# Kernel tuning notes

Hardware: AMD Instinct MI355X
Metric: run time of the kernel (lower is better)

Reference implementation:

```python
import jax, jax.numpy as jnp
import numpy as np


def _sum_matrix():
    # [69, 42] mask matrix reproducing compute_sums exactly (incl. bugs):
    # feature k = sum over cells where M[k] == 1, board flattened row-major (6x7).
    M = np.zeros((69, 42), dtype=np.float32)
    m = M.reshape(69, 6, 7)
    # 24 row window sums
    for row in range(6):
        for i in range(4):
            m[row * 4 + i, row, i:i + 4] = 1.0
    # 21 column window sums
    for col in range(7):
        for i in range(3):
            m[24 + col * 3 + i, i:i + 4, col] = 1.0
    # 12 'upward diag' sums: source sums the FULL 4x4 block of the row-flipped
    # board, i.e. original rows (2-off)..(5-off), cols col..col+3.
    for off in range(3):
        for col in range(4):
            m[45 + off * 4 + col, 2 - off:6 - off, col:col + 4] = 1.0
    # 12 'downward diag' sums: allocated but never written in source -> zeros.
    return jnp.asarray(M)


_M = _sum_matrix()  # [69, 42]


def setup_inputs() -> dict:
    key = jax.random.key(0)
    k1, k2, k3 = jax.random.split(key, 3)
    B = 524288
    game_state = jax.random.normal(k1, (B, 42), dtype=jnp.float32)
    W = jax.random.normal(k2, (7, 111), dtype=jnp.float32) * (1.0 / np.sqrt(111.0))
    b = jax.random.normal(k3, (7,), dtype=jnp.float32) * 0.01
    return {"game_state": game_state, "W": W, "b": b}


def reference(game_state, W, b):
    # sums: [B, 69] = all windowed sums as one GEMM against the mask matrix
    sums = game_state @ _M.T
    feats = jnp.concatenate([game_state, sums], axis=1)  # [B, 111]
    return feats @ W.T + b  # [B, 7]
```

## Files before the change

kernel.cpp:

```cpp
#include <hip/hip_runtime.h>


#define NFP 44

__global__ __launch_bounds__(320)
void ddqn_weff(const float* __restrict__ W, float* __restrict__ weff) {
    int tid = threadIdx.x;
    if (tid >= 7 * NFP) return;
    int j  = tid / NFP;
    int dp = tid % NFP;
    float acc = 0.0f;
    if (dp < 42) {
        acc = W[j * 111 + dp];
        int r = dp / 7, c = dp % 7;
        const float* ws = W + j * 111 + 42;
        for (int i = 0; i < 4; ++i)
            if (c >= i && c <= i + 3) acc += ws[r * 4 + i];
        for (int i = 0; i < 3; ++i)
            if (r >= i && r <= i + 3) acc += ws[24 + c * 3 + i];
        for (int off = 0; off < 3; ++off)
            for (int col = 0; col < 4; ++col)
                if (r >= 2 - off && r <= 5 - off && c >= col && c <= col + 3)
                    acc += ws[45 + off * 4 + col];
    }
    weff[tid] = acc;
}

__global__ __launch_bounds__(256)
void ddqn_main(const float* __restrict__ gs,
               const float* __restrict__ weff,
               const float* __restrict__ b,
               float* __restrict__ out) {
    __shared__ float wl[7 * NFP];
    __shared__ float bl[7];
    int t = threadIdx.x;
    for (int i = t; i < 7 * NFP; i += 256) wl[i] = weff[i];
    if (t < 7) bl[t] = b[t];
    __syncthreads();

    size_t gid = (size_t)blockIdx.x * 256 + (size_t)t;

    const float4* src = (const float4*)(gs + gid * 84);
    float xa[NFP], xb[NFP];
    #pragma unroll
    for (int i = 0; i < 21; ++i) {
        float4 v = src[i];
        float vv[4] = {v.x, v.y, v.z, v.w};
        #pragma unroll
        for (int q = 0; q < 4; ++q) {
            int f = i * 4 + q;
            if (f < 42) xa[f] = vv[q];
            else        xb[f - 42] = vv[q];
        }
    }
    xa[42] = xa[43] = 0.0f;
    xb[42] = xb[43] = 0.0f;

    float acc0[7], acc1[7];
    #pragma unroll
    for (int j = 0; j < 7; ++j) { acc0[j] = bl[j]; acc1[j] = bl[j]; }

    #pragma unroll
    for (int d = 0; d < NFP; d += 4) {
        #pragma unroll
        for (int j = 0; j < 7; ++j) {
            const float4 w = *(const float4*)&wl[j * NFP + d];
            acc0[j] += xa[d] * w.x + xa[d + 1] * w.y + xa[d + 2] * w.z + xa[d + 3] * w.w;
            acc1[j] += xb[d] * w.x + xb[d + 1] * w.y + xb[d + 2] * w.z + xb[d + 3] * w.w;
        }
    }

    float2* o = (float2*)(out + gid * 14);
    o[0] = make_float2(acc0[0], acc0[1]);
    o[1] = make_float2(acc0[2], acc0[3]);
    o[2] = make_float2(acc0[4], acc0[5]);
    o[3] = make_float2(acc0[6], acc1[0]);
    o[4] = make_float2(acc1[1], acc1[2]);
    o[5] = make_float2(acc1[3], acc1[4]);
    o[6] = make_float2(acc1[5], acc1[6]);
}

extern "C" void kernel_launch(void* const* d_in, const int* in_sizes, int n_in,
                              void* d_out, int out_size, void* d_ws, size_t ws_size,
                              hipStream_t stream) {
    const float* gs = (const float*)d_in[0];
    const float* W  = (const float*)d_in[1];
    const float* b  = (const float*)d_in[2];
    float* out  = (float*)d_out;
    float* weff = (float*)d_ws;

    ddqn_weff<<<dim3(1), dim3(320), 0, stream>>>(W, weff);

    int B = in_sizes[0] / 42;
    int nthreads = B / 2;
    ddqn_main<<<dim3(nthreads / 256), dim3(256), 0, stream>>>(gs, weff, b, out);
}
```

Measured before the change: 160.4 us.

## Stage input rows through padded LDS tile for coalesced loads, one row per thread

The main kernel now loads a 128-row tile of the input with fully coalesced scalar loads into padded shared memory, then each thread reads its own row from LDS. Previously each thread handled two rows through strided float4 global loads. Weights are read straight from global memory (uniform, likely scalar loads) instead of being staged in shared memory. The aim is better global-load coalescing, at the cost of an extra LDS round trip, scalar 7-float output stores, and small 128-thread blocks.

```diff
diff --git a/kernel.cpp b/kernel.cpp
--- a/kernel.cpp
+++ b/kernel.cpp
@@ -1,83 +1,67 @@
 #include <hip/hip_runtime.h>
 
 
-#define NFP 44
+#define TILE_ROWS 128
+#define ROW_PAD   43
 
 __global__ __launch_bounds__(320)
 void ddqn_weff(const float* __restrict__ W, float* __restrict__ weff) {
     int tid = threadIdx.x;
-    if (tid >= 7 * NFP) return;
-    int j  = tid / NFP;
-    int dp = tid % NFP;
-    float acc = 0.0f;
-    if (dp < 42) {
-        acc = W[j * 111 + dp];
-        int r = dp / 7, c = dp % 7;
-        const float* ws = W + j * 111 + 42;
-        for (int i = 0; i < 4; ++i)
-            if (c >= i && c <= i + 3) acc += ws[r * 4 + i];
-        for (int i = 0; i < 3; ++i)
-            if (r >= i && r <= i + 3) acc += ws[24 + c * 3 + i];
-        for (int off = 0; off < 3; ++off)
-            for (int col = 0; col < 4; ++col)
-                if (r >= 2 - off && r <= 5 - off && c >= col && c <= col + 3)
-                    acc += ws[45 + off * 4 + col];
-    }
-    weff[tid] = acc;
+    if (tid >= 7 * 42) return;
+    int j = tid / 42;
+    int d = tid % 42;
+    float acc = W[j * 111 + d];
+    int r = d / 7, c = d % 7;
+    const float* ws = W + j * 111 + 42;
+    for (int i = 0; i < 4; ++i)
+        if (c >= i && c <= i + 3) acc += ws[r * 4 + i];
+    for (int i = 0; i < 3; ++i)
+        if (r >= i && r <= i + 3) acc += ws[24 + c * 3 + i];
+    for (int off = 0; off < 3; ++off)
+        for (int col = 0; col < 4; ++col)
+            if (r >= 2 - off && r <= 5 - off && c >= col && c <= col + 3)
+                acc += ws[45 + off * 4 + col];
+    weff[j * 42 + d] = acc;
 }
 
-__global__ __launch_bounds__(256)
+__global__ __launch_bounds__(TILE_ROWS)
 void ddqn_main(const float* __restrict__ gs,
                const float* __restrict__ weff,
                const float* __restrict__ b,
                float* __restrict__ out) {
-    __shared__ float wl[7 * NFP];
-    __shared__ float bl[7];
-    int t = threadIdx.x;
-    for (int i = t; i < 7 * NFP; i += 256) wl[i] = weff[i];
-    if (t < 7) bl[t] = b[t];
+    __shared__ float tile[TILE_ROWS * ROW_PAD];
+    const int t = threadIdx.x;
+
+    const float* src = gs + (size_t)blockIdx.x * (TILE_ROWS * 42);
+    int row = t / 42;
+    int col = t - row * 42;
+    #pragma unroll
+    for (int k = 0; k < 42; ++k) {
+        tile[row * ROW_PAD + col] = src[k * TILE_ROWS + t];
+        row += 3; col += 2;
+        if (col >= 42) { col -= 42; row += 1; }
+    }
     __syncthreads();
 
-    size_t gid = (size_t)blockIdx.x * 256 + (size_t)t;
+    float x[42];
+    #pragma unroll
+    for (int d = 0; d < 42; ++d) x[d] = tile[t * ROW_PAD + d];
 
-    const float4* src = (const float4*)(gs + gid * 84);
-    float xa[NFP], xb[NFP];
+    float acc[7];
     #pragma unroll
-    for (int i = 0; i < 21; ++i) {
-        float4 v = src[i];
-        float vv[4] = {v.x, v.y, v.z, v.w};
-        #pragma unroll
-        for (int q = 0; q < 4; ++q) {
-            int f = i * 4 + q;
-            if (f < 42) xa[f] = vv[q];
-            else        xb[f - 42] = vv[q];
-        }
-    }
-    xa[42] = xa[43] = 0.0f;
-    xb[42] = xb[43] = 0.0f;
-
-    float acc0[7], acc1[7];
-    #pragma unroll
-    for (int j = 0; j < 7; ++j) { acc0[j] = bl[j]; acc1[j] = bl[j]; }
+    for (int j = 0; j < 7; ++j) acc[j] = b[j];
 
     #pragma unroll
-    for (int d = 0; d < NFP; d += 4) {
+    for (int d = 0; d < 42; ++d) {
         #pragma unroll
-        for (int j = 0; j < 7; ++j) {
-            const float4 w = *(const float4*)&wl[j * NFP + d];
-            acc0[j] += xa[d] * w.x + xa[d + 1] * w.y + xa[d + 2] * w.z + xa[d + 3] * w.w;
-            acc1[j] += xb[d] * w.x + xb[d + 1] * w.y + xb[d + 2] * w.z + xb[d + 3] * w.w;
-        }
+        for (int j = 0; j < 7; ++j)
+            acc[j] = fmaf(x[d], weff[j * 42 + d], acc[j]);
     }
 
-    float2* o = (float2*)(out + gid * 14);
-    o[0] = make_float2(acc0[0], acc0[1]);
-    o[1] = make_float2(acc0[2], acc0[3]);
-    o[2] = make_float2(acc0[4], acc0[5]);
-    o[3] = make_float2(acc0[6], acc1[0]);
-    o[4] = make_float2(acc1[1], acc1[2]);
-    o[5] = make_float2(acc1[3], acc1[4]);
-    o[6] = make_float2(acc1[5], acc1[6]);
+    size_t gid = (size_t)blockIdx.x * TILE_ROWS + t;
+    float* o = out + gid * 7;
+    #pragma unroll
+    for (int j = 0; j < 7; ++j) o[j] = acc[j];
 }
 
 extern "C" void kernel_launch(void* const* d_in, const int* in_sizes, int n_in,
@@ -92,6 +76,5 @@
     ddqn_weff<<<dim3(1), dim3(320), 0, stream>>>(W, weff);
 
     int B = in_sizes[0] / 42;
-    int nthreads = B / 2;
-    ddqn_main<<<dim3(nthreads / 256), dim3(256), 0, stream>>>(gs, weff, b, out);
+    ddqn_main<<<dim3(B / TILE_ROWS), dim3(TILE_ROWS), 0, stream>>>(gs, weff, b, out);
 }
```

New measurement: 141.0 us. 12.1% less time.
